# Optimization experiments

Measured on AMD Instinct MI355X. Metric: run time of the kernel, lower is better.

Reference implementation:

```python
import jax, jax.numpy as jnp
import numpy as np

IN_F = 4096
OUT_F = 4096
BW = 8
RNG_LEN = 2 ** BW  # 256


def _sobol_1d(bw):
    # 1-D Sobol sequence == van der Corput (bit-reversed) integers in [0, 2^bw),
    # matching UnarySim's RNG(bitwidth, 1, 'Sobol') table.
    n = 2 ** bw
    idx = np.arange(n, dtype=np.int64)
    rev = np.zeros(n, dtype=np.int64)
    for b in range(bw):
        rev |= ((idx >> b) & 1) << (bw - 1 - b)
    return rev.astype(np.float32)


def setup_inputs() -> dict:
    key = jax.random.key(0)
    k1, k2, k3, k4, k5, k6 = jax.random.split(key, 6)
    # unary (bit-serial) input bits for one clock cycle, batch=1
    x = jax.random.randint(k1, (1, IN_F), 0, 2).astype(jnp.float32)
    # SourceGen output: integer comparison thresholds in [0, 2^bw), stored as float
    buf_wght = jax.random.randint(k2, (OUT_F, IN_F), 0, RNG_LEN).astype(jnp.float32)
    buf_bias = jax.random.randint(k3, (OUT_F,), 0, RNG_LEN).astype(jnp.float32)
    rng = jnp.asarray(_sobol_1d(BW))  # [256] Sobol table
    # persistent BSGen index state (mid-stream snapshot, values in [0, 256))
    rng_wght_idx = jax.random.randint(k4, (OUT_F, IN_F), 0, RNG_LEN).astype(jnp.int64)
    rng_bias_idx = jax.random.randint(k5, (OUT_F,), 0, RNG_LEN).astype(jnp.int64)
    rng_wght_idx_inv = jax.random.randint(k6, (OUT_F, IN_F), 0, RNG_LEN).astype(jnp.int64)
    # persistent output accumulator (broadcast to [1, out] after first call)
    acc = jnp.zeros((1, OUT_F), dtype=jnp.float32)
    acc_bound = jnp.full((1,), float(IN_F + 1), dtype=jnp.float32)  # in_features + 1 (bias)
    return {"x": x, "buf_wght": buf_wght, "buf_bias": buf_bias, "rng": rng,
            "acc": acc, "acc_bound": acc_bound,
            "rng_wght_idx": rng_wght_idx, "rng_bias_idx": rng_bias_idx,
            "rng_wght_idx_inv": rng_wght_idx_inv}


def reference(x, buf_wght, buf_bias, rng, acc, acc_bound,
              rng_wght_idx, rng_bias_idx, rng_wght_idx_inv):
    L = rng.shape[0]
    # BSGen: regenerate binarized weight/bias bits via indexed gather + compare
    w_bit = (buf_wght >= rng[rng_wght_idx % L]).astype(jnp.float32)      # [out, in]
    b_bit = (buf_bias >= rng[rng_bias_idx % L]).astype(jnp.float32)      # [out]
    kernel_out = x @ w_bit.T + b_bit                                     # [1, out]
    # bipolar inverse path: inverted bits applied to inverted input
    w_bit_inv = 1.0 - (buf_wght >= rng[rng_wght_idx_inv % L]).astype(jnp.float32)
    kernel_out_inv = (1.0 - x) @ w_bit_inv.T                             # [1, out]
    # scaled accumulate-and-threshold
    acc_new = acc + kernel_out + kernel_out_inv
    out = (acc_new >= acc_bound).astype(jnp.float32)                     # [1, out]
    return out
```

## Files before the change

kernel.cpp:

```cpp
#include <hip/hip_runtime.h>


constexpr int IN_F  = 4096;
constexpr int OUT_F = 4096;

__global__ __launch_bounds__(256, 4) void unary_linear_kernel(
    const float* __restrict__ x,
    const float* __restrict__ buf_wght,
    const float* __restrict__ buf_bias,
    const float* __restrict__ acc,
    const float* __restrict__ acc_bound,
    const int*   __restrict__ rng_wght_idx,
    const int*   __restrict__ rng_bias_idx,
    const int*   __restrict__ rng_wght_idx_inv,
    float*       __restrict__ out)
{
    const int wave = threadIdx.x >> 6;
    const int lane = threadIdx.x & 63;
    const int row  = (blockIdx.x << 2) + wave;

    const float* __restrict__ wrow = buf_wght         + (size_t)row * IN_F;
    const int*   __restrict__ irow = rng_wght_idx     + (size_t)row * IN_F;
    const int*   __restrict__ vrow = rng_wght_idx_inv + (size_t)row * IN_F;

    float sum = 0.0f;

    #pragma unroll
    for (int c = 0; c < IN_F / 256; ++c) {
        const int base = (c * 64 + lane) * 4;
        const float4 w  = *reinterpret_cast<const float4*>(wrow + base);
        const int4   ii = *reinterpret_cast<const int4*>(irow + base);
        const int4   vi = *reinterpret_cast<const int4*>(vrow + base);
        const float4 xv = *reinterpret_cast<const float4*>(x + base);

        {
            const float r  = (float)(__brev((unsigned)ii.x) >> 24);
            const float ri = (float)(__brev((unsigned)vi.x) >> 24);
            const float bit  = (w.x >= r)  ? 1.0f : 0.0f;
            const float bitv = (w.x >= ri) ? 0.0f : 1.0f;
            sum += (xv.x != 0.0f) ? bit : bitv;
        }
        {
            const float r  = (float)(__brev((unsigned)ii.y) >> 24);
            const float ri = (float)(__brev((unsigned)vi.y) >> 24);
            const float bit  = (w.y >= r)  ? 1.0f : 0.0f;
            const float bitv = (w.y >= ri) ? 0.0f : 1.0f;
            sum += (xv.y != 0.0f) ? bit : bitv;
        }
        {
            const float r  = (float)(__brev((unsigned)ii.z) >> 24);
            const float ri = (float)(__brev((unsigned)vi.z) >> 24);
            const float bit  = (w.z >= r)  ? 1.0f : 0.0f;
            const float bitv = (w.z >= ri) ? 0.0f : 1.0f;
            sum += (xv.z != 0.0f) ? bit : bitv;
        }
        {
            const float r  = (float)(__brev((unsigned)ii.w) >> 24);
            const float ri = (float)(__brev((unsigned)vi.w) >> 24);
            const float bit  = (w.w >= r)  ? 1.0f : 0.0f;
            const float bitv = (w.w >= ri) ? 0.0f : 1.0f;
            sum += (xv.w != 0.0f) ? bit : bitv;
        }
    }

    #pragma unroll
    for (int off = 32; off > 0; off >>= 1)
        sum += __shfl_down(sum, off);

    if (lane == 0) {
        const float rb = (float)(__brev((unsigned)rng_bias_idx[row]) >> 24);
        const float b_bit = (buf_bias[row] >= rb) ? 1.0f : 0.0f;
        const float total = acc[row] + sum + b_bit;
        out[row] = (total >= acc_bound[0]) ? 1.0f : 0.0f;
    }
}

extern "C" void kernel_launch(void* const* d_in, const int* in_sizes, int n_in,
                              void* d_out, int out_size, void* d_ws, size_t ws_size,
                              hipStream_t stream)
{
    const float* x         = (const float*)d_in[0];
    const float* buf_wght  = (const float*)d_in[1];
    const float* buf_bias  = (const float*)d_in[2];
    const float* acc       = (const float*)d_in[4];
    const float* acc_bound = (const float*)d_in[5];
    const int*   rwi       = (const int*)d_in[6];
    const int*   rbi       = (const int*)d_in[7];
    const int*   rwii      = (const int*)d_in[8];
    float* out = (float*)d_out;

    dim3 grid(OUT_F / 4);
    dim3 block(256);
    hipLaunchKernelGGL(unary_linear_kernel, grid, block, 0, stream,
                       x, buf_wght, buf_bias, acc, acc_bound,
                       rwi, rbi, rwii, out);
}
```

Baseline: 207.9 us.

## Assign one block per output row with cross-wave shared-memory reduction

Each 256-thread block now handles a single output row instead of four rows (one per wave). The four waves each cover a quarter of the row, and their partial sums are combined through shared memory behind a barrier. The grid grows fourfold, and the occupancy hint in launch_bounds rises from 4 to 8. The aim is more memory-level parallelism and shorter per-thread loops on a bandwidth-bound streaming kernel, at the cost of a block-level sync and more block launches.

```diff
diff --git a/kernel.cpp b/kernel.cpp
--- a/kernel.cpp
+++ b/kernel.cpp
@@ -4,7 +4,7 @@
 constexpr int IN_F  = 4096;
 constexpr int OUT_F = 4096;
 
-__global__ __launch_bounds__(256, 4) void unary_linear_kernel(
+__global__ __launch_bounds__(256, 8) void unary_linear_kernel(
     const float* __restrict__ x,
     const float* __restrict__ buf_wght,
     const float* __restrict__ buf_bias,
@@ -15,9 +15,10 @@
     const int*   __restrict__ rng_wght_idx_inv,
     float*       __restrict__ out)
 {
-    const int wave = threadIdx.x >> 6;
-    const int lane = threadIdx.x & 63;
-    const int row  = (blockIdx.x << 2) + wave;
+    const int row  = blockIdx.x;
+    const int tid  = threadIdx.x;
+    const int wave = tid >> 6;
+    const int lane = tid & 63;
 
     const float* __restrict__ wrow = buf_wght         + (size_t)row * IN_F;
     const int*   __restrict__ irow = rng_wght_idx     + (size_t)row * IN_F;
@@ -26,8 +27,8 @@
     float sum = 0.0f;
 
     #pragma unroll
-    for (int c = 0; c < IN_F / 256; ++c) {
-        const int base = (c * 64 + lane) * 4;
+    for (int i = 0; i < 4; ++i) {
+        const int base = (i * 256 + tid) * 4;
         const float4 w  = *reinterpret_cast<const float4*>(wrow + base);
         const int4   ii = *reinterpret_cast<const int4*>(irow + base);
         const int4   vi = *reinterpret_cast<const int4*>(vrow + base);
@@ -36,30 +37,26 @@
         {
             const float r  = (float)(__brev((unsigned)ii.x) >> 24);
             const float ri = (float)(__brev((unsigned)vi.x) >> 24);
-            const float bit  = (w.x >= r)  ? 1.0f : 0.0f;
-            const float bitv = (w.x >= ri) ? 0.0f : 1.0f;
-            sum += (xv.x != 0.0f) ? bit : bitv;
+            sum += (xv.x != 0.0f) ? ((w.x >= r) ? 1.0f : 0.0f)
+                                  : ((w.x >= ri) ? 0.0f : 1.0f);
         }
         {
             const float r  = (float)(__brev((unsigned)ii.y) >> 24);
             const float ri = (float)(__brev((unsigned)vi.y) >> 24);
-            const float bit  = (w.y >= r)  ? 1.0f : 0.0f;
-            const float bitv = (w.y >= ri) ? 0.0f : 1.0f;
-            sum += (xv.y != 0.0f) ? bit : bitv;
+            sum += (xv.y != 0.0f) ? ((w.y >= r) ? 1.0f : 0.0f)
+                                  : ((w.y >= ri) ? 0.0f : 1.0f);
         }
         {
             const float r  = (float)(__brev((unsigned)ii.z) >> 24);
             const float ri = (float)(__brev((unsigned)vi.z) >> 24);
-            const float bit  = (w.z >= r)  ? 1.0f : 0.0f;
-            const float bitv = (w.z >= ri) ? 0.0f : 1.0f;
-            sum += (xv.z != 0.0f) ? bit : bitv;
+            sum += (xv.z != 0.0f) ? ((w.z >= r) ? 1.0f : 0.0f)
+                                  : ((w.z >= ri) ? 0.0f : 1.0f);
         }
         {
             const float r  = (float)(__brev((unsigned)ii.w) >> 24);
             const float ri = (float)(__brev((unsigned)vi.w) >> 24);
-            const float bit  = (w.w >= r)  ? 1.0f : 0.0f;
-            const float bitv = (w.w >= ri) ? 0.0f : 1.0f;
-            sum += (xv.w != 0.0f) ? bit : bitv;
+            sum += (xv.w != 0.0f) ? ((w.w >= r) ? 1.0f : 0.0f)
+                                  : ((w.w >= ri) ? 0.0f : 1.0f);
         }
     }
 
@@ -67,10 +64,14 @@
     for (int off = 32; off > 0; off >>= 1)
         sum += __shfl_down(sum, off);
 
-    if (lane == 0) {
+    __shared__ float wsum[4];
+    if (lane == 0) wsum[wave] = sum;
+    __syncthreads();
+
+    if (tid == 0) {
         const float rb = (float)(__brev((unsigned)rng_bias_idx[row]) >> 24);
         const float b_bit = (buf_bias[row] >= rb) ? 1.0f : 0.0f;
-        const float total = acc[row] + sum + b_bit;
+        const float total = acc[row] + wsum[0] + wsum[1] + wsum[2] + wsum[3] + b_bit;
         out[row] = (total >= acc_bound[0]) ? 1.0f : 0.0f;
     }
 }
@@ -89,7 +90,7 @@
     const int*   rwii      = (const int*)d_in[8];
     float* out = (float*)d_out;
 
-    dim3 grid(OUT_F / 4);
+    dim3 grid(OUT_F);
     dim3 block(256);
     hipLaunchKernelGGL(unary_linear_kernel, grid, block, 0, stream,
                        x, buf_wght, buf_bias, acc, acc_bound,
```

Result: no change. 211.1 us (+1.6%).
